# Kernel optimization log

Measured on AMD Instinct MI355X. Metric: run time of the kernel, lower is better.

Reference implementation:

```python
import jax, jax.numpy as jnp
import numpy as np


def setup_inputs() -> dict:
    key = jax.random.key(0)
    ks = jax.random.split(key, 6)
    N, C, H = 3072, 2048, 16
    hd = C // H  # 128
    x = jax.random.normal(ks[0], (N, C), dtype=jnp.float32)
    # rotary frequencies as cos/sin of per-position angles (real view of complex freqs_cis)
    inv_freq = 1.0 / (10000.0 ** (np.arange(0, hd, 2, dtype=np.float32) / hd))  # [hd/2]
    angles = jnp.arange(N, dtype=jnp.float32)[:, None] * jnp.asarray(inv_freq)[None, :]  # [N, hd/2]
    freqs_cos = jnp.cos(angles)
    freqs_sin = jnp.sin(angles)
    qkv_w = jax.random.normal(ks[1], (3 * C, C), dtype=jnp.float32) * 0.02
    qkv_b = jnp.zeros((3 * C,), dtype=jnp.float32)
    proj_w = jax.random.normal(ks[2], (C, C), dtype=jnp.float32) * 0.02
    proj_b = jnp.zeros((C,), dtype=jnp.float32)
    cu_seqlens = jnp.array([0, 768, 1536, 2304, 3072], dtype=jnp.int32)
    return {
        "x": x, "freqs_cos": freqs_cos, "freqs_sin": freqs_sin,
        "qkv_w": qkv_w, "qkv_b": qkv_b, "proj_w": proj_w, "proj_b": proj_b,
        "cu_seqlens": cu_seqlens, "max_seqlen": 768,
    }


def _rope(t, cos, sin):
    # t: [H, N, hd]; interpret consecutive pairs as complex, multiply by freqs_cis
    tr, ti = t[..., 0::2], t[..., 1::2]              # [H, N, hd/2]
    o_re = tr * cos - ti * sin
    o_im = tr * sin + ti * cos
    return jnp.stack([o_re, o_im], axis=-1).reshape(t.shape)


def reference(x, freqs_cos, freqs_sin, qkv_w, qkv_b, proj_w, proj_b, cu_seqlens, max_seqlen):
    N, C = x.shape
    hd = freqs_cos.shape[-1] * 2
    H = C // hd
    qkv = (x @ qkv_w.T + qkv_b).reshape(N, 3, H, hd).transpose(1, 2, 0, 3)  # [3, H, N, hd]
    q, k, v = qkv[0], qkv[1], qkv[2]
    q = _rope(q, freqs_cos, freqs_sin)
    k = _rope(k, freqs_cos, freqs_sin)
    # varlen attention: block-diagonal mask from cu_seqlens segment membership
    seg = jnp.searchsorted(cu_seqlens[1:], jnp.arange(N), side="right")  # [N]
    mask = seg[:, None] == seg[None, :]                                  # [N, N]
    scale = 1.0 / np.sqrt(hd).astype(np.float32)
    scores = jnp.einsum("hnd,hmd->hnm", q, k) * scale                    # [H, N, N]
    scores = jnp.where(mask[None], scores, jnp.finfo(scores.dtype).min)
    probs = jax.nn.softmax(scores, axis=-1)
    out = jnp.einsum("hnm,hmd->hnd", probs, v)                           # [H, N, hd]
    out = out.transpose(1, 0, 2).reshape(N, C)
    return out @ proj_w.T + proj_b
```

## Files before the change

kernel.cpp:

```cpp
#include <hip/hip_runtime.h>
#include <stdint.h>

#define N_TOK  3072
#define C_DIM  2048
#define K3C    6144
#define NHEAD  16
#define HD     128
#define SEGLEN 768

typedef __attribute__((ext_vector_type(8))) short  short8;
typedef __attribute__((ext_vector_type(4))) float  f32x4;

__device__ __forceinline__ unsigned short f2bf(float f) {
  unsigned u = __builtin_bit_cast(unsigned, f);
  u += 0x7FFFu + ((u >> 16) & 1u);
  return (unsigned short)(u >> 16);
}
__device__ __forceinline__ float bf2f(unsigned short h) {
  unsigned u = ((unsigned)h) << 16;
  return __builtin_bit_cast(float, u);
}
__device__ __forceinline__ void gload_lds16(const void* g, void* l) {
  __builtin_amdgcn_global_load_lds(
      (const __attribute__((address_space(1))) unsigned int*)g,
      (__attribute__((address_space(3))) unsigned int*)l, 16, 0, 0);
}

#define XB_ELEMS    (3072L*2048L)
#define WQKV_ELEMS  (6144L*2048L)
#define WPROJ_ELEMS (2048L*2048L)
__global__ __launch_bounds__(256) void cast_bf16_kernel(
    const float* __restrict__ x, const float* __restrict__ wqkv,
    const float* __restrict__ wproj, unsigned short* __restrict__ xb,
    unsigned short* __restrict__ wqkvb, unsigned short* __restrict__ wprojb) {
  long t = (long)blockIdx.x * 256 + threadIdx.x;
  long i = t * 8;
  const float* src; unsigned short* dst; long off;
  if (i < XB_ELEMS)                   { src = x;     dst = xb;     off = i; }
  else if (i < XB_ELEMS + WQKV_ELEMS) { src = wqkv;  dst = wqkvb;  off = i - XB_ELEMS; }
  else                                { src = wproj; dst = wprojb; off = i - XB_ELEMS - WQKV_ELEMS; }
  f32x4 a = *(const f32x4*)(src + off);
  f32x4 b = *(const f32x4*)(src + off + 4);
  short8 o;
  #pragma unroll
  for (int k = 0; k < 4; ++k) { o[k] = (short)f2bf(a[k]); o[k+4] = (short)f2bf(b[k]); }
  *(short8*)(dst + off) = o;
}

#define VM4 asm volatile("s_waitcnt vmcnt(4)" ::: "memory");
#define VM0 asm volatile("s_waitcnt vmcnt(0)" ::: "memory");

#define STAGE(buf, mat, h, t, BASE) do { \
  const unsigned short* _src = (BASE) + (size_t)(tid & 255) * (size_t)K_ \
                               + (size_t)((t)*64 + ((h)*4 + (tid >> 8))*8); \
  char* _l = ldsB + ((((buf)*2 + (mat))*8 + (h)*4) * 4096) + wv*1024; \
  gload_lds16(_src,      _l); \
  gload_lds16(_src + 16, _l + 8192); \
} while (0)

#define PHASE(buf, kk, mh, LOADB, STAGES, WAIT) do { \
  short8 aF[4]; \
  _Pragma("unroll") \
  for (int j = 0; j < 4; ++j) \
    aF[j] = *(const short8*)&sH[buf][0][(kk)*4 + lh][wr*128 + ((mh)*4 + j)*16 + lr][0]; \
  if (LOADB) { \
    _Pragma("unroll") \
    for (int n = 0; n < 4; ++n) \
      bF[n] = *(const short8*)&sH[buf][1][(kk)*4 + lh][wc*64 + n*16 + lr][0]; \
  } \
  STAGES \
  __builtin_amdgcn_s_barrier(); \
  asm volatile("s_waitcnt lgkmcnt(0)" ::: "memory"); \
  __builtin_amdgcn_sched_barrier(0); \
  __builtin_amdgcn_s_setprio(1); \
  _Pragma("unroll") \
  for (int j = 0; j < 4; ++j) { \
    _Pragma("unroll") \
    for (int n = 0; n < 4; ++n) \
      acc[(mh)*4 + j][n] = __builtin_amdgcn_mfma_f32_16x16x32_bf16(aF[j], bF[n], acc[(mh)*4 + j][n], 0, 0, 0); \
  } \
  __builtin_amdgcn_s_setprio(0); \
  __builtin_amdgcn_sched_barrier(0); \
  WAIT \
  __builtin_amdgcn_s_barrier(); \
} while (0)

template<bool OUTF32>
__global__ __launch_bounds__(512, 2) void gemm8p(
    const unsigned short* __restrict__ A, const unsigned short* __restrict__ B,
    const float* __restrict__ bias, void* __restrict__ Cout,
    int N, int K_) {
  __shared__ __align__(16) unsigned short sH[2][2][8][256][8];
  char* ldsB = (char*)&sH[0][0][0][0][0];
  const int tid = threadIdx.x;
  const int wv = tid >> 6, l = tid & 63, lr = l & 15, lh = l >> 4;
  const int wr = wv >> 2, wc = wv & 3;
  const long row0 = (long)blockIdx.y * 256;
  const long col0 = (long)blockIdx.x * 256;
  const unsigned short* Ab = A + row0 * K_;
  const unsigned short* Bb = B + col0 * K_;
  f32x4 acc[8][4] = {};
  short8 bF[4];

  STAGE(0,0,0, 0, Ab); STAGE(0,1,0, 0, Bb); STAGE(0,0,1, 0, Ab); STAGE(0,1,1, 0, Bb);
  STAGE(1,0,0, 1, Ab); STAGE(1,1,0, 1, Bb);
  VM4
  __builtin_amdgcn_s_barrier();

  const int NITER = K_ >> 7;
  int t0 = 0;
  #pragma unroll 1
  for (int it = 0; it < NITER - 1; ++it, t0 += 2) {
    PHASE(0,0,0, 1, STAGE(1,0,1, t0+1, Ab);, );
    PHASE(0,0,1, 0, STAGE(1,1,1, t0+1, Bb);, );
    PHASE(0,1,0, 1, STAGE(0,0,0, t0+2, Ab);, );
    PHASE(0,1,1, 0, STAGE(0,1,0, t0+2, Bb);, VM4);
    PHASE(1,0,0, 1, STAGE(0,0,1, t0+2, Ab);, );
    PHASE(1,0,1, 0, STAGE(0,1,1, t0+2, Bb);, );
    PHASE(1,1,0, 1, STAGE(1,0,0, t0+3, Ab);, );
    PHASE(1,1,1, 0, STAGE(1,1,0, t0+3, Bb);, VM4);
  }
  PHASE(0,0,0, 1, STAGE(1,0,1, t0+1, Ab);, );
  PHASE(0,0,1, 0, STAGE(1,1,1, t0+1, Bb);, );
  PHASE(0,1,0, 1, , );
  PHASE(0,1,1, 0, , VM0);
  PHASE(1,0,0, 1, , );
  PHASE(1,0,1, 0, , );
  PHASE(1,1,0, 1, , );
  PHASE(1,1,1, 0, , );

  #pragma unroll
  for (int n = 0; n < 4; ++n) {
    const long col = col0 + wc*64 + n*16 + lr;
    const float bv = bias[col];
    #pragma unroll
    for (int m = 0; m < 8; ++m) {
      const long rb = row0 + wr*128 + m*16 + lh*4;
      #pragma unroll
      for (int r = 0; r < 4; ++r) {
        float val = acc[m][n][r] + bv;
        if constexpr (OUTF32) ((float*)Cout)[(rb + r)*N + col] = val;
        else ((unsigned short*)Cout)[(rb + r)*N + col] = f2bf(val);
      }
    }
  }
}

__global__ __launch_bounds__(256) void rope_kernel(
    unsigned short* __restrict__ qkv, const float* __restrict__ fcos,
    const float* __restrict__ fsin) {
  long t = (long)blockIdx.x * 256 + threadIdx.x;
  int n  = (int)(t >> 9);
  int col = (int)(t & 511) * 8;
  int j0 = (col & 127) >> 1;
  unsigned short* p = qkv + (long)n * K3C + col;
  short8 v = *(short8*)p;
  f32x4 vc = *(const f32x4*)(fcos + n*64 + j0);
  f32x4 vs = *(const f32x4*)(fsin + n*64 + j0);
  short8 o;
  #pragma unroll
  for (int i = 0; i < 4; ++i) {
    float re = bf2f((unsigned short)v[2*i]);
    float im = bf2f((unsigned short)v[2*i+1]);
    float c = vc[i], s = vs[i];
    o[2*i]   = (short)f2bf(re*c - im*s);
    o[2*i+1] = (short)f2bf(re*s + im*c);
  }
  *(short8*)p = o;
}

__global__ __launch_bounds__(256) void transpose_v_kernel(
    const unsigned short* __restrict__ qkv, unsigned short* __restrict__ vT) {
  __shared__ unsigned short sT[64*64];
  int bidx = blockIdx.x;
  const int nb = (bidx % 48) * 64; bidx /= 48;
  const int db = (bidx & 1) * 64;  bidx >>= 1;
  const int h  = bidx;
  const int tid = threadIdx.x;
  #pragma unroll
  for (int p = 0; p < 2; ++p) {
    int ch = tid + p*256;
    int row = ch >> 3, c8 = ch & 7;
    f32x4 val = *(const f32x4*)(qkv + (long)(nb + row)*K3C + 4096 + h*HD + db + c8*8);
    int off = (row*128 + c8*16) ^ ((row & 7) << 4);
    *(f32x4*)((char*)sT + off) = val;
  }
  __syncthreads();
  #pragma unroll
  for (int p = 0; p < 2; ++p) {
    int ch = tid + p*256;
    int drow = ch >> 3, nc = ch & 7;
    short8 tv;
    #pragma unroll
    for (int j = 0; j < 8; ++j) {
      int nn = nc*8 + j;
      int off = (nn*128 + drow*2) ^ ((nn & 7) << 4);
      tv[j] = *(const short*)((const char*)sT + off);
    }
    *(short8*)(vT + ((long)h*HD + db + drow)*N_TOK + nb + nc*8) = tv;
  }
}

__global__ __launch_bounds__(256) void attn_kernel(
    const unsigned short* __restrict__ qkv, const unsigned short* __restrict__ vT,
    unsigned short* __restrict__ attb) {
  __shared__ unsigned short sK [64*128];
  __shared__ unsigned short sVT[128*64];
  __shared__ unsigned short sP [4][16*72];
  const int tid = threadIdx.x;
  const int w = tid >> 6, l = tid & 63, lr = l & 15, lh = l >> 4;
  int bidx = blockIdx.x;
  const int qt = bidx % 12; bidx /= 12;
  const int h  = bidx & 15; bidx >>= 4;
  const int s  = bidx;
  const int n0 = s*SEGLEN + qt*64;
  const float scale = 0.08838834764831845f;
  const float LOG2E = 1.4426950408889634f;

  short8 aq[4];
  {
    const unsigned short* qrow = qkv + (long)(n0 + w*16 + lr)*K3C + h*HD;
    #pragma unroll
    for (int c = 0; c < 4; ++c) aq[c] = *(const short8*)(qrow + c*32 + lh*8);
  }
  f32x4 o[8] = {};
  float m_r[4] = {-1e30f, -1e30f, -1e30f, -1e30f};
  float l_r[4] = {0.f, 0.f, 0.f, 0.f};

  for (int kt = 0; kt < 12; ++kt) {
    const int kb = s*SEGLEN + kt*64;
    __syncthreads();
    #pragma unroll
    for (int p = 0; p < 4; ++p) {
      int ch = (p*4 + w)*64 + l;
      int key = ch >> 4;
      int kc  = (ch & 15) ^ (key & 7);
      gload_lds16(qkv + (long)(kb + key)*K3C + C_DIM + h*HD + kc*8,
                  (char*)sK + (size_t)(p*4 + w)*1024);
      int d   = ch >> 3;
      int kc2 = (ch & 7) ^ (d & 7);
      gload_lds16(vT + ((long)h*HD + d)*N_TOK + kb + kc2*8,
                  (char*)sVT + (size_t)(p*4 + w)*1024);
    }
    __syncthreads();

    f32x4 sacc[4] = {};
    #pragma unroll
    for (int kd = 0; kd < 4; ++kd)
      #pragma unroll
      for (int kf = 0; kf < 4; ++kf) {
        int key = kf*16 + lr;
        int off = (key*256 + kd*64 + lh*16) ^ ((key & 7) << 4);
        short8 bk = *(const short8*)((const char*)sK + off);
        sacc[kf] = __builtin_amdgcn_mfma_f32_16x16x32_bf16(aq[kd], bk, sacc[kf], 0, 0, 0);
      }

    float alpha[4];
    #pragma unroll
    for (int r = 0; r < 4; ++r) {
      float v0 = fmaxf(fmaxf(sacc[0][r], sacc[1][r]), fmaxf(sacc[2][r], sacc[3][r]));
      #pragma unroll
      for (int sh = 1; sh < 16; sh <<= 1) v0 = fmaxf(v0, __shfl_xor(v0, sh, 64));
      float pm = v0 * scale;
      float mn = fmaxf(m_r[r], pm);
      alpha[r] = __builtin_exp2f((m_r[r] - mn) * LOG2E);
      m_r[r] = mn;
    }
    float rsum[4] = {0.f, 0.f, 0.f, 0.f};
    #pragma unroll
    for (int kf = 0; kf < 4; ++kf)
      #pragma unroll
      for (int r = 0; r < 4; ++r) {
        float pv = __builtin_exp2f((sacc[kf][r]*scale - m_r[r]) * LOG2E);
        rsum[r] += pv;
        sP[w][(lh*4 + r)*72 + kf*16 + lr] = f2bf(pv);
      }
    #pragma unroll
    for (int r = 0; r < 4; ++r) {
      float t = rsum[r];
      #pragma unroll
      for (int sh = 1; sh < 16; sh <<= 1) t += __shfl_xor(t, sh, 64);
      l_r[r] = l_r[r]*alpha[r] + t;
    }
    #pragma unroll
    for (int nf = 0; nf < 8; ++nf)
      #pragma unroll
      for (int r = 0; r < 4; ++r) o[nf][r] *= alpha[r];

    #pragma unroll
    for (int ks = 0; ks < 2; ++ks) {
      short8 ap = *(const short8*)&sP[w][lr*72 + ks*32 + lh*8];
      #pragma unroll
      for (int nf = 0; nf < 8; ++nf) {
        int d = nf*16 + lr;
        int off = (d*128 + ks*64 + lh*16) ^ ((d & 7) << 4);
        short8 bv = *(const short8*)((const char*)sVT + off);
        o[nf] = __builtin_amdgcn_mfma_f32_16x16x32_bf16(ap, bv, o[nf], 0, 0, 0);
      }
    }
  }

  #pragma unroll
  for (int r = 0; r < 4; ++r) {
    float inv = 1.0f / l_r[r];
    int n = n0 + w*16 + lh*4 + r;
    unsigned short* orow = attb + (long)n*C_DIM + h*HD;
    #pragma unroll
    for (int nf = 0; nf < 8; ++nf) orow[nf*16 + lr] = f2bf(o[nf][r] * inv);
  }
}

extern "C" void kernel_launch(void* const* d_in, const int* in_sizes, int n_in,
                              void* d_out, int out_size, void* d_ws, size_t ws_size,
                              hipStream_t stream) {
  (void)in_sizes; (void)n_in; (void)out_size; (void)ws_size;
  const float* x      = (const float*)d_in[0];
  const float* fcos   = (const float*)d_in[1];
  const float* fsin   = (const float*)d_in[2];
  const float* qkv_w  = (const float*)d_in[3];
  const float* qkv_b  = (const float*)d_in[4];
  const float* proj_w = (const float*)d_in[5];
  const float* proj_b = (const float*)d_in[6];

  char* ws = (char*)d_ws;
  unsigned short* xb     = (unsigned short*)(ws + 0L);
  unsigned short* wqkvb  = (unsigned short*)(ws + 12582912L);
  unsigned short* wprojb = (unsigned short*)(ws + 37748736L);
  unsigned short* qkvb   = (unsigned short*)(ws + 46137344L);
  unsigned short* vT     = (unsigned short*)(ws + 83886080L);
  unsigned short* attb   = xb;

  cast_bf16_kernel<<<11264, 256, 0, stream>>>(x, qkv_w, proj_w, xb, wqkvb, wprojb);
  gemm8p<false><<<dim3(24, 12), 512, 0, stream>>>(xb, wqkvb, qkv_b, qkvb, 6144, 2048);
  rope_kernel<<<6144, 256, 0, stream>>>(qkvb, fcos, fsin);
  transpose_v_kernel<<<1536, 256, 0, stream>>>(qkvb, vT);
  attn_kernel<<<768, 256, 0, stream>>>(qkvb, vT, attb);
  gemm8p<true><<<dim3(8, 12), 512, 0, stream>>>(attb, wprojb, proj_b, d_out, 2048, 2048);
}
```

Baseline: 478.4 us.

## Replace 256x256 8-wave GEMM tile with 128x128 4-wave tile

Both GEMMs switch from a 256x256 output tile with 512 threads to a 128x128 tile with 256 threads. The LDS staging, phase schedule and accumulator layout are rewritten to match. This raises the block count (1152 and 384 blocks instead of 288 and 96), which fills all CUs and evens out the tail, especially for the small projection GEMM. In exchange, each loaded byte is reused less, so more global and LDS traffic is needed per FLOP.

```diff
diff --git a/kernel.cpp b/kernel.cpp
--- a/kernel.cpp
+++ b/kernel.cpp
@@ -50,34 +50,32 @@
 #define VM4 asm volatile("s_waitcnt vmcnt(4)" ::: "memory");
 #define VM0 asm volatile("s_waitcnt vmcnt(0)" ::: "memory");
 
-#define STAGE(buf, mat, h, t, BASE) do { \
-  const unsigned short* _src = (BASE) + (size_t)(tid & 255) * (size_t)K_ \
-                               + (size_t)((t)*64 + ((h)*4 + (tid >> 8))*8); \
-  char* _l = ldsB + ((((buf)*2 + (mat))*8 + (h)*4) * 4096) + wv*1024; \
-  gload_lds16(_src,      _l); \
-  gload_lds16(_src + 16, _l + 8192); \
+#define STAGE_H(buf, mat, h, t, BASE) do { \
+  const unsigned short* _s0 = (BASE) + (size_t)l        * (size_t)K_ \
+                              + (size_t)((t)*64 + ((h)*4 + wv)*8); \
+  char* _d0 = ldsB + ((((buf)*2 + (mat))*8 + (h)*4 + wv) * 128) * 16; \
+  gload_lds16(_s0,                      _d0); \
+  gload_lds16(_s0 + (size_t)64 * K_,    _d0 + 1024); \
 } while (0)
 
-#define PHASE(buf, kk, mh, LOADB, STAGES, WAIT) do { \
-  short8 aF[4]; \
+#define PHASE4(buf, kk, STAGES, WAIT) do { \
+  short8 aF[4], bF[4]; \
   _Pragma("unroll") \
-  for (int j = 0; j < 4; ++j) \
-    aF[j] = *(const short8*)&sH[buf][0][(kk)*4 + lh][wr*128 + ((mh)*4 + j)*16 + lr][0]; \
-  if (LOADB) { \
-    _Pragma("unroll") \
-    for (int n = 0; n < 4; ++n) \
-      bF[n] = *(const short8*)&sH[buf][1][(kk)*4 + lh][wc*64 + n*16 + lr][0]; \
-  } \
+  for (int m = 0; m < 4; ++m) \
+    aF[m] = *(const short8*)&sH[buf][0][(kk)*4 + lh][wr*64 + m*16 + lr][0]; \
+  _Pragma("unroll") \
+  for (int n = 0; n < 4; ++n) \
+    bF[n] = *(const short8*)&sH[buf][1][(kk)*4 + lh][wc*64 + n*16 + lr][0]; \
   STAGES \
   __builtin_amdgcn_s_barrier(); \
   asm volatile("s_waitcnt lgkmcnt(0)" ::: "memory"); \
   __builtin_amdgcn_sched_barrier(0); \
   __builtin_amdgcn_s_setprio(1); \
   _Pragma("unroll") \
-  for (int j = 0; j < 4; ++j) { \
+  for (int m = 0; m < 4; ++m) { \
     _Pragma("unroll") \
     for (int n = 0; n < 4; ++n) \
-      acc[(mh)*4 + j][n] = __builtin_amdgcn_mfma_f32_16x16x32_bf16(aF[j], bF[n], acc[(mh)*4 + j][n], 0, 0, 0); \
+      acc[m][n] = __builtin_amdgcn_mfma_f32_16x16x32_bf16(aF[m], bF[n], acc[m][n], 0, 0, 0); \
   } \
   __builtin_amdgcn_s_setprio(0); \
   __builtin_amdgcn_sched_barrier(0); \
@@ -86,24 +84,24 @@
 } while (0)
 
 template<bool OUTF32>
-__global__ __launch_bounds__(512, 2) void gemm8p(
+__global__ __launch_bounds__(256, 2) void gemm128(
     const unsigned short* __restrict__ A, const unsigned short* __restrict__ B,
     const float* __restrict__ bias, void* __restrict__ Cout,
     int N, int K_) {
-  __shared__ __align__(16) unsigned short sH[2][2][8][256][8];
+  __shared__ __align__(16) unsigned short sH[2][2][8][128][8];
   char* ldsB = (char*)&sH[0][0][0][0][0];
   const int tid = threadIdx.x;
   const int wv = tid >> 6, l = tid & 63, lr = l & 15, lh = l >> 4;
-  const int wr = wv >> 2, wc = wv & 3;
-  const long row0 = (long)blockIdx.y * 256;
-  const long col0 = (long)blockIdx.x * 256;
+  const int wr = wv >> 1, wc = wv & 1;
+  const long row0 = (long)blockIdx.y * 128;
+  const long col0 = (long)blockIdx.x * 128;
   const unsigned short* Ab = A + row0 * K_;
   const unsigned short* Bb = B + col0 * K_;
-  f32x4 acc[8][4] = {};
-  short8 bF[4];
-
-  STAGE(0,0,0, 0, Ab); STAGE(0,1,0, 0, Bb); STAGE(0,0,1, 0, Ab); STAGE(0,1,1, 0, Bb);
-  STAGE(1,0,0, 1, Ab); STAGE(1,1,0, 1, Bb);
+  f32x4 acc[4][4] = {};
+
+  STAGE_H(0,0,0, 0, Ab); STAGE_H(0,1,0, 0, Bb);
+  STAGE_H(0,0,1, 0, Ab); STAGE_H(0,1,1, 0, Bb);
+  STAGE_H(1,0,0, 1, Ab); STAGE_H(1,1,0, 1, Bb);
   VM4
   __builtin_amdgcn_s_barrier();
 
@@ -111,31 +109,23 @@
   int t0 = 0;
   #pragma unroll 1
   for (int it = 0; it < NITER - 1; ++it, t0 += 2) {
-    PHASE(0,0,0, 1, STAGE(1,0,1, t0+1, Ab);, );
-    PHASE(0,0,1, 0, STAGE(1,1,1, t0+1, Bb);, );
-    PHASE(0,1,0, 1, STAGE(0,0,0, t0+2, Ab);, );
-    PHASE(0,1,1, 0, STAGE(0,1,0, t0+2, Bb);, VM4);
-    PHASE(1,0,0, 1, STAGE(0,0,1, t0+2, Ab);, );
-    PHASE(1,0,1, 0, STAGE(0,1,1, t0+2, Bb);, );
-    PHASE(1,1,0, 1, STAGE(1,0,0, t0+3, Ab);, );
-    PHASE(1,1,1, 0, STAGE(1,1,0, t0+3, Bb);, VM4);
-  }
-  PHASE(0,0,0, 1, STAGE(1,0,1, t0+1, Ab);, );
-  PHASE(0,0,1, 0, STAGE(1,1,1, t0+1, Bb);, );
-  PHASE(0,1,0, 1, , );
-  PHASE(0,1,1, 0, , VM0);
-  PHASE(1,0,0, 1, , );
-  PHASE(1,0,1, 0, , );
-  PHASE(1,1,0, 1, , );
-  PHASE(1,1,1, 0, , );
+    PHASE4(0, 0, STAGE_H(1,0,1, t0+1, Ab); STAGE_H(1,1,1, t0+1, Bb);, );
+    PHASE4(0, 1, STAGE_H(0,0,0, t0+2, Ab); STAGE_H(0,1,0, t0+2, Bb);, VM4);
+    PHASE4(1, 0, STAGE_H(0,0,1, t0+2, Ab); STAGE_H(0,1,1, t0+2, Bb);, );
+    PHASE4(1, 1, STAGE_H(1,0,0, t0+3, Ab); STAGE_H(1,1,0, t0+3, Bb);, VM4);
+  }
+  PHASE4(0, 0, STAGE_H(1,0,1, t0+1, Ab); STAGE_H(1,1,1, t0+1, Bb);, );
+  PHASE4(0, 1, , VM0);
+  PHASE4(1, 0, , );
+  PHASE4(1, 1, , );
 
   #pragma unroll
   for (int n = 0; n < 4; ++n) {
     const long col = col0 + wc*64 + n*16 + lr;
     const float bv = bias[col];
     #pragma unroll
-    for (int m = 0; m < 8; ++m) {
-      const long rb = row0 + wr*128 + m*16 + lh*4;
+    for (int m = 0; m < 4; ++m) {
+      const long rb = row0 + wr*64 + m*16 + lh*4;
       #pragma unroll
       for (int r = 0; r < 4; ++r) {
         float val = acc[m][n][r] + bv;
@@ -331,9 +321,9 @@
   unsigned short* attb   = xb;
 
   cast_bf16_kernel<<<11264, 256, 0, stream>>>(x, qkv_w, proj_w, xb, wqkvb, wprojb);
-  gemm8p<false><<<dim3(24, 12), 512, 0, stream>>>(xb, wqkvb, qkv_b, qkvb, 6144, 2048);
+  gemm128<false><<<dim3(48, 24), 256, 0, stream>>>(xb, wqkvb, qkv_b, qkvb, 6144, 2048);
   rope_kernel<<<6144, 256, 0, stream>>>(qkvb, fcos, fsin);
   transpose_v_kernel<<<1536, 256, 0, stream>>>(qkvb, vT);
   attn_kernel<<<768, 256, 0, stream>>>(qkvb, vT, attb);
-  gemm8p<true><<<dim3(8, 12), 512, 0, stream>>>(attb, wprojb, proj_b, d_out, 2048, 2048);
-}
+  gemm128<true><<<dim3(16, 24), 256, 0, stream>>>(attb, wprojb, proj_b, d_out, 2048, 2048);
+}
```

After: 443.3 us. 1.08x faster.
